# Optimization experiments

Hardware: AMD Instinct MI355X
Metric: run time of the kernel (lower is better)

Reference implementation:

```python
import jax, jax.numpy as jnp
import numpy as np


def _quant_dequant_rowwise(v):
    # vector-wise absmax int8 quantization along the last axis, then dequant.
    # Exactly reproduces dequantized result of the int8 GEMM operand:
    # Cx = round(v/s) clipped to [-127,127]; dq = Cx * s.
    s = jnp.max(jnp.abs(v), axis=-1, keepdims=True) / 127.0
    s = jnp.maximum(s, 1e-8)
    q = jnp.clip(jnp.round(v / s), -127.0, 127.0)
    return q * s


def setup_inputs() -> dict:
    key = jax.random.key(0)
    k1, k2, k3 = jax.random.split(key, 3)
    B, S, K, N = 4, 2048, 4096, 4096
    x = jax.random.normal(k1, (B, S, K), dtype=jnp.float32)
    # amplify a few feature columns so |col| exceeds the 6.0 outlier threshold,
    # exercising the LLM.int8() mixed-precision decomposition path
    x = x.at[..., ::256].multiply(10.0)
    W = jax.random.normal(k2, (N, K), dtype=jnp.float32) * 0.02
    bias = jax.random.normal(k3, (N,), dtype=jnp.float32) * 0.01
    return {"x": x, "W": W, "bias": bias, "threshold": 6}


def reference(x, W, bias, threshold):
    # LLM.int8() matmul with outlier decomposition (bnb.matmul semantics):
    #  1. columns of x whose absmax > threshold are outliers -> fp16/fp32 path
    #  2. remaining x columns + full W are vector-wise int8 quantized, int8 GEMM,
    #     dequant with per-row scales (exactly equal to dq(x) @ dq(W).T)
    #  3. out = int8-part + x_outlier @ W_outlier.T + bias
    thr = jnp.asarray(threshold, dtype=x.dtype)
    B_shape = x.shape[:-1]
    K = x.shape[-1]
    x2 = x.reshape(-1, K)                                   # [M, K]
    colmax = jnp.max(jnp.abs(x2), axis=0)                   # [K]
    out_mask = (colmax > thr).astype(x.dtype)               # 1.0 on outlier cols
    x_int = x2 * (1.0 - out_mask)                           # zero outlier cols
    dq_x = _quant_dequant_rowwise(x_int)                    # [M, K]
    dq_w = _quant_dequant_rowwise(W)                        # [N, K]
    out = dq_x @ dq_w.T                                     # int8 GEMM, dequantized
    out = out + (x2 * out_mask) @ (W * out_mask).T          # fp outlier GEMM
    out = out + bias
    return out.reshape(*B_shape, W.shape[0])
```

## Files before the change

kernel.cpp:

```cpp
#include <hip/hip_runtime.h>

typedef unsigned short u16;
typedef unsigned char u8;
typedef unsigned int u32;
typedef __attribute__((ext_vector_type(4))) float f32x4;
typedef __attribute__((ext_vector_type(16))) float f32x16;
typedef __attribute__((ext_vector_type(8))) __bf16 bf16x8;
typedef __attribute__((ext_vector_type(4))) int i32x4;
typedef __attribute__((ext_vector_type(16))) int i32x16;

__device__ __forceinline__ u16 f2bf(float f) {
  u32 u = __float_as_uint(f);
  u32 r = (u + 0x7fffu + ((u >> 16) & 1u)) >> 16;
  return (u16)r;
}

__device__ __forceinline__ float load_thr(const int* p) {
  int iv = *p;
  float fv = __int_as_float(iv);
  if (fv >= 1.0f && fv <= 1.0e6f) return fv;
  return (float)iv;
}

__device__ __forceinline__ void gload_lds16(const void* g, void* l) {
  __builtin_amdgcn_global_load_lds(
      (const __attribute__((address_space(1))) void*)g,
      (__attribute__((address_space(3))) void*)l, 16, 0, 0);
}

__global__ void k_init_cm(u32* cm, int K) {
  int i = blockIdx.x * 256 + threadIdx.x;
  if (i < K) cm[i] = 0u;
}

__global__ __launch_bounds__(256) void k_colmax(const float* __restrict__ x,
                                                u32* __restrict__ cm, int M,
                                                int K, int rpb) {
  int c4 = blockIdx.x * 256 + threadIdx.x;
  int r0 = blockIdx.y * rpb;
  int r1 = r0 + rpb;
  if (r1 > M) r1 = M;
  f32x4 mx = {0.f, 0.f, 0.f, 0.f};
  for (int r = r0; r < r1; ++r) {
    f32x4 v = *(const f32x4*)&x[(size_t)r * K + (size_t)c4 * 4];
#pragma unroll
    for (int i = 0; i < 4; ++i) mx[i] = fmaxf(mx[i], fabsf(v[i]));
  }
#pragma unroll
  for (int i = 0; i < 4; ++i)
    atomicMax(&cm[c4 * 4 + i], __float_as_uint(mx[i]));
}

__global__ void k_ocols(const u32* __restrict__ cm, const int* __restrict__ thr_i,
                        int K, int* __restrict__ meta) {
  int lane = threadIdx.x;
  float thr = load_thr(thr_i);
  const float* cmf = (const float*)cm;
  int per = K >> 6;
  int base = lane * per;
  int c = 0;
  for (int i = 0; i < per; ++i) c += (cmf[base + i] > thr) ? 1 : 0;
  int inc = c;
  for (int off = 1; off < 64; off <<= 1) {
    int t = __shfl_up(inc, off);
    if (lane >= off) inc += t;
  }
  int excl = inc - c;
  int total = __shfl(inc, 63);
  if (lane == 0) meta[0] = total < 64 ? total : 64;
  int idx = excl;
  for (int i = 0; i < per; ++i) {
    if (cmf[base + i] > thr) {
      if (idx < 64) meta[1 + idx] = base + i;
      idx++;
    }
  }
  for (int j = total + lane; j < 64; j += 64) meta[1 + j] = -1;
}

__global__ __launch_bounds__(256) void k_quant8(
    const float* __restrict__ src, const u32* __restrict__ cm,
    const int* __restrict__ thr_i, const int* __restrict__ meta,
    char* __restrict__ qdst, float* __restrict__ sdst, u16* __restrict__ odst,
    int K, int zero_outlier) {
  int row = blockIdx.x;
  int tid = threadIdx.x;
  float thr = load_thr(thr_i);
  const float* sr = src + (size_t)row * K;
  const float* cmf = (const float*)cm;

  float v[16];
  u32 omask = 0;
  float lmax = 0.f;
#pragma unroll
  for (int j = 0; j < 4; ++j) {
    int c4 = j * 256 + tid;
    f32x4 val = *(const f32x4*)&sr[c4 * 4];
    f32x4 cv = *(const f32x4*)&cmf[c4 * 4];
#pragma unroll
    for (int i = 0; i < 4; ++i) {
      float xv = val[i];
      v[j * 4 + i] = xv;
      bool is_out = cv[i] > thr;
      if (is_out) omask |= 1u << (j * 4 + i);
      if (!is_out || !zero_outlier) lmax = fmaxf(lmax, fabsf(xv));
    }
  }
  float m = lmax;
#pragma unroll
  for (int off = 32; off >= 1; off >>= 1) m = fmaxf(m, __shfl_down(m, off));
  __shared__ float red[4];
  int lane = tid & 63, wv = tid >> 6;
  if (lane == 0) red[wv] = m;
  __syncthreads();
  float rm = fmaxf(fmaxf(red[0], red[1]), fmaxf(red[2], red[3]));
  float s = fmaxf(rm / 127.0f, 1e-8f);

  u32* qt = (u32*)qdst;
  size_t rowpart = (size_t)(row >> 5) * (K >> 5) * 256 + (size_t)(row & 31) * 8;
  u32 wxor = ((row >> 2) & 1) << 2;
#pragma unroll
  for (int j = 0; j < 4; ++j) {
    int c4 = j * 256 + tid;
    u32 pk = 0;
#pragma unroll
    for (int i = 0; i < 4; ++i) {
      float xv = v[j * 4 + i];
      int iq;
      if (zero_outlier && (omask & (1u << (j * 4 + i)))) {
        iq = 0;
      } else {
        float q = rintf(xv / s);
        q = fminf(fmaxf(q, -127.f), 127.f);
        iq = (int)q;
      }
      pk |= ((u32)(u8)(char)iq) << (8 * i);
    }
    qt[rowpart + (size_t)(c4 >> 3) * 256 + ((c4 & 7) ^ wxor)] = pk;
  }
  if (tid == 0) sdst[row] = s;
  if (tid < 64) {
    int n_out = meta[0];
    int oc = meta[1 + tid];
    u16 ov = 0;
    if (tid < n_out && oc >= 0) ov = f2bf(sr[oc]);
    odst[(size_t)row * 64 + tid] = ov;
  }
}

__global__ __launch_bounds__(512, 4) void k_gemm_i8(
    const char* __restrict__ qx, const char* __restrict__ qw,
    const float* __restrict__ sx, const float* __restrict__ sw,
    const float* __restrict__ bias, const char* __restrict__ xo,
    const char* __restrict__ wo, float* __restrict__ out, int M, int N,
    int K) {
  extern __shared__ char lds_raw[];
  int tid = threadIdx.x;
  int lane = tid & 63, wave = tid >> 6;
  int wm = wave >> 2, wn = wave & 3;

  int nwg = gridDim.x, bid = blockIdx.x;
  int swzb = (bid & 7) * (nwg >> 3) + (bid >> 3);
  int nbn = N >> 8;
  int bm = swzb / nbn, bn = swzb % nbn;
  int r0 = bm << 7, c0 = bn << 8;
  int K32 = K >> 5;
  int lbyte = (lane & 31) * 32 + ((((lane >> 5) ^ (lane >> 2)) & 1) << 4);

  const char* bptr[4];
  int bg[4];
#pragma unroll
  for (int i = 0; i < 4; ++i) {
    int g = tid + i * 512;
    int b = g >> 6;
    int nb = b >> 2, kb = b & 3;
    bptr[i] = qw + ((size_t)((c0 >> 5) + nb) * K32 + kb) * 1024 + (g & 63) * 16;
    bg[i] = g;
  }
#define STAGE_B(bufp, kt)                                                     \
  {                                                                           \
    _Pragma("unroll") for (int i = 0; i < 4; ++i)                             \
        gload_lds16(bptr[i] + ((size_t)((kt) >> 5) << 10), (bufp) + bg[i] * 16); \
  }

  const char* abase0 = qx + ((size_t)((r0 >> 5) + wm * 2) * K32 << 10) + lbyte;
  const char* abase1 = abase0 + ((size_t)K32 << 10);
#define LDA2(aq, kt, ksA, ksB)                                                \
  {                                                                           \
    aq[0] = *(const i32x4*)(abase0 + ((size_t)(((kt) >> 5) + (ksA)) << 10));  \
    aq[1] = *(const i32x4*)(abase1 + ((size_t)(((kt) >> 5) + (ksA)) << 10));  \
    aq[2] = *(const i32x4*)(abase0 + ((size_t)(((kt) >> 5) + (ksB)) << 10));  \
    aq[3] = *(const i32x4*)(abase1 + ((size_t)(((kt) >> 5) + (ksB)) << 10));  \
  }

#define BFR2(bq, bufp, ksA, ksB)                                              \
  {                                                                           \
    bq[0] = *(const i32x4*)((bufp) + (((wn * 2 + 0) * 4 + (ksA)) << 10) + lbyte); \
    bq[1] = *(const i32x4*)((bufp) + (((wn * 2 + 1) * 4 + (ksA)) << 10) + lbyte); \
    bq[2] = *(const i32x4*)((bufp) + (((wn * 2 + 0) * 4 + (ksB)) << 10) + lbyte); \
    bq[3] = *(const i32x4*)((bufp) + (((wn * 2 + 1) * 4 + (ksB)) << 10) + lbyte); \
  }

#define MFI(q, nf, av, bv)                                                    \
  asm volatile("v_mfma_i32_32x32x32_i8 %0, %1, %2, %0"                        \
               : "+v"(acc[q][nf])                                             \
               : "v"(av), "v"(bv))

#define MH(aq, bq)                                                            \
  {                                                                           \
    __builtin_amdgcn_s_setprio(1);                                            \
    MFI(0, 0, aq[0], bq[0]);                                                  \
    MFI(0, 1, aq[0], bq[1]);                                                  \
    MFI(1, 0, aq[1], bq[0]);                                                  \
    MFI(1, 1, aq[1], bq[1]);                                                  \
    MFI(0, 0, aq[2], bq[2]);                                                  \
    MFI(0, 1, aq[2], bq[3]);                                                  \
    MFI(1, 0, aq[3], bq[2]);                                                  \
    MFI(1, 1, aq[3], bq[3]);                                                  \
    __builtin_amdgcn_s_setprio(0);                                            \
  }

#define TILE(bufc, bufn, kt, ktn)                                             \
  {                                                                           \
    i32x4 aq[4], bq[4];                                                       \
    LDA2(aq, kt, 0, 1);                                                       \
    STAGE_B(bufn, ktn);                                                       \
    BFR2(bq, bufc, 0, 1);                                                     \
    asm volatile("s_waitcnt vmcnt(4)" ::: "memory");                          \
    asm volatile("s_waitcnt lgkmcnt(0)" ::: "memory");                        \
    MH(aq, bq);                                                               \
    LDA2(aq, kt, 2, 3);                                                       \
    BFR2(bq, bufc, 2, 3);                                                     \
    asm volatile("s_waitcnt vmcnt(0)" ::: "memory");                          \
    asm volatile("s_waitcnt lgkmcnt(0)" ::: "memory");                        \
    MH(aq, bq);                                                               \
    __builtin_amdgcn_s_barrier();                                             \
  }

  char* buf0 = lds_raw;
  char* buf1 = lds_raw + 32768;
  i32x16 acc[2][2] = {};

  STAGE_B(buf0, 0);
  asm volatile("s_waitcnt vmcnt(0)" ::: "memory");
  __builtin_amdgcn_s_barrier();

  int nit = K / 256;
  for (int it = 0; it < nit; ++it) {
    int kt0 = it * 256;
    int kt1 = it * 256 + 128;
    int kt2 = it * 256 + 256;
    kt2 = (kt2 < K) ? kt2 : 0;
    TILE(buf0, buf1, kt0, kt1);
    TILE(buf1, buf0, kt1, kt2);
  }

#pragma unroll
  for (int i = 0; i < 2; ++i) {
    int g = tid + i * 512;
    int rw = g >> 3;
    int cb = ((g & 7) ^ (rw & 7)) << 4;
    gload_lds16(xo + (size_t)(r0 + rw) * 128 + cb, lds_raw + g * 16);
  }
#pragma unroll
  for (int i = 0; i < 4; ++i) {
    int g = tid + i * 512;
    int rw = g >> 3;
    int cb = ((g & 7) ^ (rw & 7)) << 4;
    gload_lds16(wo + (size_t)(c0 + rw) * 128 + cb, lds_raw + 16384 + g * 16);
  }

  f32x16 facc[2][2];
  float swv[2], bv[2];
#pragma unroll
  for (int nf = 0; nf < 2; ++nf) {
    swv[nf] = sw[c0 + wn * 64 + nf * 32 + (lane & 31)];
    bv[nf] = bias[c0 + wn * 64 + nf * 32 + (lane & 31)];
  }
#pragma unroll
  for (int q = 0; q < 2; ++q) {
    int gmb = r0 + wm * 64 + q * 32 + 4 * (lane >> 5);
    f32x4 s4a = *(const f32x4*)&sx[gmb];
    f32x4 s4b = *(const f32x4*)&sx[gmb + 8];
    f32x4 s4c = *(const f32x4*)&sx[gmb + 16];
    f32x4 s4d = *(const f32x4*)&sx[gmb + 24];
#pragma unroll
    for (int reg = 0; reg < 16; ++reg) {
      float sxv = (reg < 4) ? s4a[reg & 3]
                : (reg < 8) ? s4b[reg & 3]
                : (reg < 12) ? s4c[reg & 3] : s4d[reg & 3];
#pragma unroll
      for (int nf = 0; nf < 2; ++nf)
        facc[q][nf][reg] = (float)acc[q][nf][reg] * sxv * swv[nf];
    }
  }

  asm volatile("s_waitcnt vmcnt(0)" ::: "memory");
  __builtin_amdgcn_s_barrier();

#pragma unroll
  for (int ks = 0; ks < 4; ++ks) {
    bf16x8 ob[2];
#pragma unroll
    for (int nf = 0; nf < 2; ++nf) {
      int rn = wn * 64 + nf * 32 + (lane & 31);
      ob[nf] = *(const bf16x8*)(lds_raw + 16384 + rn * 128 +
                                (((ks * 2 + (lane >> 5)) ^ (rn & 7)) << 4));
    }
#pragma unroll
    for (int q = 0; q < 2; ++q) {
      int rl = wm * 64 + q * 32 + (lane & 31);
      bf16x8 oa = *(const bf16x8*)(lds_raw + rl * 128 +
                                   (((ks * 2 + (lane >> 5)) ^ (rl & 7)) << 4));
#pragma unroll
      for (int nf = 0; nf < 2; ++nf)
        facc[q][nf] = __builtin_amdgcn_mfma_f32_32x32x16_bf16(
            oa, ob[nf], facc[q][nf], 0, 0, 0);
    }
  }

#pragma unroll
  for (int q = 0; q < 2; ++q) {
#pragma unroll
    for (int reg = 0; reg < 16; ++reg) {
      int gm = r0 + wm * 64 + q * 32 + (reg & 3) + 8 * (reg >> 2) +
               4 * (lane >> 5);
      float* orow = out + (size_t)gm * N + c0 + wn * 64 + (lane & 31);
#pragma unroll
      for (int nf = 0; nf < 2; ++nf)
        orow[nf * 32] = facc[q][nf][reg] + bv[nf];
    }
  }
}

extern "C" void kernel_launch(void* const* d_in, const int* in_sizes, int n_in,
                              void* d_out, int out_size, void* d_ws,
                              size_t ws_size, hipStream_t stream) {
  const float* x = (const float*)d_in[0];
  const float* W = (const float*)d_in[1];
  const float* bias = (const float*)d_in[2];
  const int* thr = (const int*)d_in[3];
  float* out = (float*)d_out;

  int N = in_sizes[2];
  int K = in_sizes[1] / N;
  int M = in_sizes[0] / K;

  char* ws = (char*)d_ws;
  u32* cm = (u32*)ws;
  int* meta = (int*)(ws + 16384);
  float* sx = (float*)(ws + 32768);
  float* sw = (float*)(ws + 32768 + (size_t)M * 4);
  char* xo = ws + 32768 + (size_t)(M + N) * 4;
  char* wo = xo + (size_t)M * 128;
  char* qx = wo + (size_t)N * 128;
  char* qw = qx + (size_t)M * K;

  k_init_cm<<<dim3((K + 255) / 256), dim3(256), 0, stream>>>(cm, K);

  {
    int gx = K / 1024;
    int gy = 128;
    int rpb = (M + gy - 1) / gy;
    k_colmax<<<dim3(gx, gy), dim3(256), 0, stream>>>(x, cm, M, K, rpb);
  }

  k_ocols<<<dim3(1), dim3(64), 0, stream>>>(cm, thr, K, meta);

  k_quant8<<<dim3(M), dim3(256), 0, stream>>>(x, cm, thr, meta, qx, sx,
                                              (u16*)xo, K, 1);
  k_quant8<<<dim3(N), dim3(256), 0, stream>>>(W, cm, thr, meta, qw, sw,
                                              (u16*)wo, K, 0);

  (void)hipFuncSetAttribute((const void*)k_gemm_i8,
                            hipFuncAttributeMaxDynamicSharedMemorySize,
                            65536);
  int nwg = (M / 128) * (N / 256);
  k_gemm_i8<<<dim3(nwg), dim3(512), 65536, stream>>>(qx, qw, sx, sw, bias,
                                                     xo, wo, out, M, N, K);
}
```

Baseline: 288.4 us.

## Stage both A and B tiles through LDS with 64-wide K double buffering

The int8 GEMM main loop now copies both the activation (A) and weight (B) tiles into LDS with direct global-to-LDS loads, instead of reading A straight from global memory into registers. The K step shrinks from 128 to 64, the double-buffer footprint drops from 64 KB to 48 KB, and the MFMA calls move from inline asm to the compiler builtin. The XOR swizzle on the quantized layout and on the LDS read offsets is removed, which may bring back LDS bank conflicts. The smaller K step also doubles the number of barriers per K, with less work between them to hide load latency.

```diff
diff --git a/kernel.cpp b/kernel.cpp
--- a/kernel.cpp
+++ b/kernel.cpp
@@ -118,7 +118,6 @@
 
   u32* qt = (u32*)qdst;
   size_t rowpart = (size_t)(row >> 5) * (K >> 5) * 256 + (size_t)(row & 31) * 8;
-  u32 wxor = ((row >> 2) & 1) << 2;
 #pragma unroll
   for (int j = 0; j < 4; ++j) {
     int c4 = j * 256 + tid;
@@ -136,7 +135,7 @@
       }
       pk |= ((u32)(u8)(char)iq) << (8 * i);
     }
-    qt[rowpart + (size_t)(c4 >> 3) * 256 + ((c4 & 7) ^ wxor)] = pk;
+    qt[rowpart + (size_t)(c4 >> 3) * 256 + (c4 & 7)] = pk;
   }
   if (tid == 0) sdst[row] = s;
   if (tid < 64) {
@@ -165,95 +164,84 @@
   int bm = swzb / nbn, bn = swzb % nbn;
   int r0 = bm << 7, c0 = bn << 8;
   int K32 = K >> 5;
-  int lbyte = (lane & 31) * 32 + ((((lane >> 5) ^ (lane >> 2)) & 1) << 4);
-
-  const char* bptr[4];
-  int bg[4];
-#pragma unroll
-  for (int i = 0; i < 4; ++i) {
-    int g = tid + i * 512;
-    int b = g >> 6;
-    int nb = b >> 2, kb = b & 3;
-    bptr[i] = qw + ((size_t)((c0 >> 5) + nb) * K32 + kb) * 1024 + (g & 63) * 16;
-    bg[i] = g;
-  }
-#define STAGE_B(bufp, kt)                                                     \
+  int lbyte = (lane & 31) * 32 + (lane >> 5) * 16;
+
+  const char* asrc;
+  {
+    int b = tid >> 6, mb = b >> 1, kb = b & 1;
+    asrc = qx + ((size_t)((r0 >> 5) + mb) * K32 + kb) * 1024 + (tid & 63) * 16;
+  }
+  const char* bsrc0;
+  const char* bsrc1;
+  {
+    int g = tid, b = g >> 6, nb = b >> 1, kb = b & 1;
+    bsrc0 = qw + ((size_t)((c0 >> 5) + nb) * K32 + kb) * 1024 + (g & 63) * 16;
+    g = tid + 512; b = g >> 6; nb = b >> 1; kb = b & 1;
+    bsrc1 = qw + ((size_t)((c0 >> 5) + nb) * K32 + kb) * 1024 + (g & 63) * 16;
+  }
+
+#define BUF0 (lds_raw)
+#define BUF1 (lds_raw + 24576)
+#define STAGE(bufp, kt)                                                       \
   {                                                                           \
-    _Pragma("unroll") for (int i = 0; i < 4; ++i)                             \
-        gload_lds16(bptr[i] + ((size_t)((kt) >> 5) << 10), (bufp) + bg[i] * 16); \
-  }
-
-  const char* abase0 = qx + ((size_t)((r0 >> 5) + wm * 2) * K32 << 10) + lbyte;
-  const char* abase1 = abase0 + ((size_t)K32 << 10);
-#define LDA2(aq, kt, ksA, ksB)                                                \
-  {                                                                           \
-    aq[0] = *(const i32x4*)(abase0 + ((size_t)(((kt) >> 5) + (ksA)) << 10));  \
-    aq[1] = *(const i32x4*)(abase1 + ((size_t)(((kt) >> 5) + (ksA)) << 10));  \
-    aq[2] = *(const i32x4*)(abase0 + ((size_t)(((kt) >> 5) + (ksB)) << 10));  \
-    aq[3] = *(const i32x4*)(abase1 + ((size_t)(((kt) >> 5) + (ksB)) << 10));  \
-  }
-
-#define BFR2(bq, bufp, ksA, ksB)                                              \
-  {                                                                           \
-    bq[0] = *(const i32x4*)((bufp) + (((wn * 2 + 0) * 4 + (ksA)) << 10) + lbyte); \
-    bq[1] = *(const i32x4*)((bufp) + (((wn * 2 + 1) * 4 + (ksA)) << 10) + lbyte); \
-    bq[2] = *(const i32x4*)((bufp) + (((wn * 2 + 0) * 4 + (ksB)) << 10) + lbyte); \
-    bq[3] = *(const i32x4*)((bufp) + (((wn * 2 + 1) * 4 + (ksB)) << 10) + lbyte); \
-  }
+    gload_lds16(asrc + (((kt) >> 5) << 10), (bufp) + tid * 16);               \
+    gload_lds16(bsrc0 + (((kt) >> 5) << 10), (bufp) + 8192 + tid * 16);       \
+    gload_lds16(bsrc1 + (((kt) >> 5) << 10),                                  \
+                (bufp) + 8192 + (tid + 512) * 16);                            \
+  }
+
+#define LDAI(dst, bufp, q, ks)                                                \
+  dst = *(const i32x4*)((bufp) + (((wm * 2 + (q)) * 2 + (ks)) << 10) + lbyte);
+#define LDBI(dst, bufp, nf, ks)                                               \
+  dst = *(const i32x4*)((bufp) + 8192 +                                       \
+                        (((wn * 2 + (nf)) * 2 + (ks)) << 10) + lbyte);
 
 #define MFI(q, nf, av, bv)                                                    \
-  asm volatile("v_mfma_i32_32x32x32_i8 %0, %1, %2, %0"                        \
-               : "+v"(acc[q][nf])                                             \
-               : "v"(av), "v"(bv))
-
-#define MH(aq, bq)                                                            \
-  {                                                                           \
-    __builtin_amdgcn_s_setprio(1);                                            \
-    MFI(0, 0, aq[0], bq[0]);                                                  \
-    MFI(0, 1, aq[0], bq[1]);                                                  \
-    MFI(1, 0, aq[1], bq[0]);                                                  \
-    MFI(1, 1, aq[1], bq[1]);                                                  \
-    MFI(0, 0, aq[2], bq[2]);                                                  \
-    MFI(0, 1, aq[2], bq[3]);                                                  \
-    MFI(1, 0, aq[3], bq[2]);                                                  \
-    MFI(1, 1, aq[3], bq[3]);                                                  \
-    __builtin_amdgcn_s_setprio(0);                                            \
-  }
+  acc[q][nf] =                                                                \
+      __builtin_amdgcn_mfma_i32_32x32x32_i8(av, bv, acc[q][nf], 0, 0, 0)
 
 #define TILE(bufc, bufn, kt, ktn)                                             \
   {                                                                           \
-    i32x4 aq[4], bq[4];                                                       \
-    LDA2(aq, kt, 0, 1);                                                       \
-    STAGE_B(bufn, ktn);                                                       \
-    BFR2(bq, bufc, 0, 1);                                                     \
-    asm volatile("s_waitcnt vmcnt(4)" ::: "memory");                          \
+    STAGE(bufn, ktn);                                                         \
+    asm volatile("s_waitcnt vmcnt(3)" ::: "memory");                          \
+    __builtin_amdgcn_s_barrier();                                             \
+    i32x4 a00, a01, a10, a11, b00, b01, b10, b11;                             \
+    LDAI(a00, bufc, 0, 0);                                                    \
+    LDAI(a01, bufc, 0, 1);                                                    \
+    LDAI(a10, bufc, 1, 0);                                                    \
+    LDAI(a11, bufc, 1, 1);                                                    \
+    LDBI(b00, bufc, 0, 0);                                                    \
+    LDBI(b01, bufc, 0, 1);                                                    \
+    LDBI(b10, bufc, 1, 0);                                                    \
+    LDBI(b11, bufc, 1, 1);                                                    \
     asm volatile("s_waitcnt lgkmcnt(0)" ::: "memory");                        \
-    MH(aq, bq);                                                               \
-    LDA2(aq, kt, 2, 3);                                                       \
-    BFR2(bq, bufc, 2, 3);                                                     \
-    asm volatile("s_waitcnt vmcnt(0)" ::: "memory");                          \
-    asm volatile("s_waitcnt lgkmcnt(0)" ::: "memory");                        \
-    MH(aq, bq);                                                               \
+    __builtin_amdgcn_s_setprio(1);                                            \
+    MFI(0, 0, a00, b00);                                                      \
+    MFI(0, 1, a00, b10);                                                      \
+    MFI(1, 0, a10, b00);                                                      \
+    MFI(1, 1, a10, b10);                                                      \
+    MFI(0, 0, a01, b01);                                                      \
+    MFI(0, 1, a01, b11);                                                      \
+    MFI(1, 0, a11, b01);                                                      \
+    MFI(1, 1, a11, b11);                                                      \
+    __builtin_amdgcn_s_setprio(0);                                            \
     __builtin_amdgcn_s_barrier();                                             \
   }
 
-  char* buf0 = lds_raw;
-  char* buf1 = lds_raw + 32768;
   i32x16 acc[2][2] = {};
 
-  STAGE_B(buf0, 0);
+  STAGE(BUF0, 0);
+
+  int NT = K >> 6;
+  for (int t = 0; t < NT; t += 2) {
+    int kt1 = (t + 1) << 6;
+    int kt2 = (t + 2) < NT ? (t + 2) << 6 : 0;
+    TILE(BUF0, BUF1, t << 6, kt1);
+    TILE(BUF1, BUF0, kt1, kt2);
+  }
+
   asm volatile("s_waitcnt vmcnt(0)" ::: "memory");
   __builtin_amdgcn_s_barrier();
-
-  int nit = K / 256;
-  for (int it = 0; it < nit; ++it) {
-    int kt0 = it * 256;
-    int kt1 = it * 256 + 128;
-    int kt2 = it * 256 + 256;
-    kt2 = (kt2 < K) ? kt2 : 0;
-    TILE(buf0, buf1, kt0, kt1);
-    TILE(buf1, buf0, kt1, kt2);
-  }
 
 #pragma unroll
   for (int i = 0; i < 2; ++i) {
@@ -374,8 +362,8 @@
 
   (void)hipFuncSetAttribute((const void*)k_gemm_i8,
                             hipFuncAttributeMaxDynamicSharedMemorySize,
-                            65536);
+                            49152);
   int nwg = (M / 128) * (N / 256);
-  k_gemm_i8<<<dim3(nwg), dim3(512), 65536, stream>>>(qx, qw, sx, sw, bias,
+  k_gemm_i8<<<dim3(nwg), dim3(512), 49152, stream>>>(qx, qw, sx, sw, bias,
                                                      xo, wo, out, M, N, K);
 }
```

Result: faster. 271.1 us (-6.0%).
